# Kernel optimization log

Hardware: AMD Instinct MI355X
Metric: run time of the kernel (lower is better)

## Reference

```python
import jax, jax.numpy as jnp
import numpy as np
from jax import lax

B, D, H, W = 4, 64, 64, 64
CH = 150


def setup_inputs() -> dict:
    key = jax.random.key(0)
    k1, k2, k3, k4 = jax.random.split(key, 4)
    image = jax.random.uniform(k1, (B, 2, D, H, W), dtype=jnp.float32)
    # PyTorch-like init scales
    h_w = jax.random.normal(k2, (CH, 1, 3, 3, 3), dtype=jnp.float32) * (1.0 / np.sqrt(27.0))
    h_b = jax.random.normal(k3, (CH,), dtype=jnp.float32) * 0.05
    p_w = jax.random.normal(k4, (1, CH, 1, 1, 1), dtype=jnp.float32) * (1.0 / np.sqrt(CH))
    return {"image": image, "h_w": h_w, "h_b": h_b, "p_w": p_w, "k": 30}


def _max_pool3(v):
    # 3x3x3 max pool, stride 1, padding 1 (torch pads with -inf for max pool)
    return lax.reduce_window(
        v, -jnp.inf, lax.max,
        window_dimensions=(1, 1, 3, 3, 3),
        window_strides=(1, 1, 1, 1, 1),
        padding=[(0, 0), (0, 0), (1, 1), (1, 1), (1, 1)])


def reference(image, h_w, h_b, p_w, k):
    x = image[:, 0:1]            # [B,1,D,H,W] occupancy
    r = image[:, 1:2]            # [B,1,D,H,W] reward
    h = lax.conv_general_dilated(
        x, h_w, window_strides=(1, 1, 1), padding="SAME",
        dimension_numbers=("NCDHW", "OIDHW", "NCDHW"))
    h = jax.nn.relu(h + h_b[None, :, None, None, None])  # [B,150,D,H,W]
    # 1x1x1 conv == channel contraction
    p = jax.nn.sigmoid(jnp.einsum("bcdhw,c->bdhw", h, p_w[0, :, 0, 0, 0])[:, None])
    v = r
    for _ in range(k):
        v = jnp.maximum(v, r + p * (_max_pool3(v) - r))
    return v
```

## Files before the change

kernel.cpp:

```cpp
#include <hip/hip_runtime.h>
#include <math.h>

#define NEG_INF (-__builtin_inff())

typedef __attribute__((ext_vector_type(8))) short short8;
typedef __attribute__((ext_vector_type(4))) float f32x4;

__device__ __forceinline__ unsigned f2bf(float f) {
    union { float f; unsigned u; } v; v.f = f;
    return (v.u + 0x7fffu + ((v.u >> 16) & 1u)) >> 16;
}

__device__ __forceinline__ float dpp_shr1(float x) {
    return __int_as_float(__builtin_amdgcn_update_dpp(
        0, __float_as_int(x), 0x111, 0xF, 0xF, true));
}
__device__ __forceinline__ float dpp_shl1(float x) {
    return __int_as_float(__builtin_amdgcn_update_dpp(
        0, __float_as_int(x), 0x101, 0xF, 0xF, true));
}

__global__ __launch_bounds__(256) void pad_kernel(
    const float* __restrict__ img, unsigned short* __restrict__ pad)
{
    int i = blockIdx.x * 256 + threadIdx.x;
    if (i >= 66 * 66 * 66) return;
    int b = blockIdx.y;
    int z = i / 4356;
    int rem = i - z * 4356;
    int y = rem / 66;
    int x = rem - y * 66;
    float v = 0.f;
    if (z >= 1 && z <= 64 && y >= 1 && y <= 64 && x >= 1 && x <= 64)
        v = img[((size_t)b << 19) + ((z - 1) << 12) + ((y - 1) << 6) + (x - 1)];
    pad[(size_t)b * 287496 + i] = (unsigned short)f2bf(v);
}

__global__ __launch_bounds__(256, 2) void gate_mfma(
    const unsigned short* __restrict__ pad,
    const float* __restrict__ hw, const float* __restrict__ hb,
    const float* __restrict__ pw, float* __restrict__ p)
{
    const int lane = threadIdx.x & 63;
    const int col  = lane & 15;
    const int q    = lane >> 4;
    const int W    = blockIdx.x * 4 + (threadIdx.x >> 6);

    int4  bfrag[10];
    float pwv[10];
    #pragma unroll
    for (int t = 0; t < 10; ++t) {
        int c = 16 * t + col;
        bool cv = c < 150;
        unsigned hv[8];
        #pragma unroll
        for (int j = 0; j < 8; ++j) {
            int k = 8 * q + j;
            float wv = 0.f;
            if (cv) {
                if (k < 27) wv = hw[c * 27 + k];
                else if (k == 27) wv = hb[c];
            }
            hv[j] = f2bf(wv);
        }
        bfrag[t] = make_int4(hv[0] | (hv[1] << 16), hv[2] | (hv[3] << 16),
                             hv[4] | (hv[5] << 16), hv[6] | (hv[7] << 16));
        pwv[t] = cv ? pw[c] : 0.f;
    }

    int offL[8]; unsigned cstA[8]; bool ldA[8];
    #pragma unroll
    for (int j = 0; j < 8; ++j) {
        int k = 8 * q + j;
        int dz = (k * 57) >> 9;
        int rem = k - 9 * dz;
        int dy = (rem * 171) >> 9;
        int dx = rem - 3 * dy;
        ldA[j]  = (k < 27);
        offL[j] = (k < 27) ? (dz * 4356 + dy * 66 + dx) : 0;
        cstA[j] = (k == 27) ? 0x3F80u : 0u;
    }

    for (int i = 0; i < 16; ++i) {
        int g   = W * 16 + i;
        int x0  = (g & 3) << 4;
        int row = g >> 2;
        int y = row & 63, zz = (row >> 6) & 63, b = row >> 12;
        int abase = b * 287496 + zz * 4356 + y * 66 + x0 + col;

        unsigned av[8];
        #pragma unroll
        for (int j = 0; j < 8; ++j) {
            unsigned v = pad[abase + offL[j]];
            av[j] = ldA[j] ? v : cstA[j];
        }
        union { int4 i4; short8 s8; } af, bfu;
        af.i4 = make_int4(av[0] | (av[1] << 16), av[2] | (av[3] << 16),
                          av[4] | (av[5] << 16), av[6] | (av[7] << 16));

        const f32x4 zero = {0.f, 0.f, 0.f, 0.f};
        f32x4 rr[10];
        #pragma unroll
        for (int t = 0; t < 10; ++t) {
            bfu.i4 = bfrag[t];
            rr[t] = __builtin_amdgcn_mfma_f32_16x16x32_bf16(af.s8, bfu.s8, zero, 0, 0, 0);
        }
        float ax = 0.f, ay = 0.f, az = 0.f, aw = 0.f;
        #pragma unroll
        for (int t = 0; t < 10; ++t) {
            ax = fmaf(pwv[t], fmaxf(rr[t].x, 0.f), ax);
            ay = fmaf(pwv[t], fmaxf(rr[t].y, 0.f), ay);
            az = fmaf(pwv[t], fmaxf(rr[t].z, 0.f), az);
            aw = fmaf(pwv[t], fmaxf(rr[t].w, 0.f), aw);
        }
        #pragma unroll
        for (int m = 1; m < 16; m <<= 1) {
            ax += __shfl_xor(ax, m);
            ay += __shfl_xor(ay, m);
            az += __shfl_xor(az, m);
            aw += __shfl_xor(aw, m);
        }
        if (col == 0) {
            float4 o;
            o.x = 1.f / (1.f + __expf(-ax));
            o.y = 1.f / (1.f + __expf(-ay));
            o.z = 1.f / (1.f + __expf(-az));
            o.w = 1.f / (1.f + __expf(-aw));
            *(float4*)(p + (b << 18) + (zz << 12) + (y << 6) + x0 + 4 * q) = o;
        }
    }
}

#define ZC 12
#define YC 16
#define PL 1024
#define ZMID 6

template<int T>
__global__ __launch_bounds__(512, 4) void prop_kernel(
    const float* __restrict__ vin, int sstride,
    const float* __restrict__ rimg,
    const float* __restrict__ pbuf,
    float* __restrict__ vout)
{
    __shared__ float S[ZC * PL];
    int blk = blockIdx.x;
    int b  = blk >> 7;
    int tz = ((blk >> 3) & 15) << 2;
    int ty = (blk & 7) << 3;

    const float* vb = vin  + (size_t)b * sstride;
    const float* rb = rimg + ((size_t)b << 19);
    const float* pb = pbuf + ((size_t)b << 18);
    float*       ob = vout + ((size_t)b << 18);

    int tid  = threadIdx.x;
    int x4   = tid & 15, x0 = x4 << 2;
    int yy   = (tid >> 4) & 15;
    int h    = tid >> 8;
    int lane = tid & 63;
    (void)lane;

    int gy = ty + yy - 4;
    bool vy = (unsigned)gy < 64u;

    {
        const float* src = vb + gy * 64 + x0;
        #pragma unroll
        for (int zi = 0; zi < 6; ++zi) {
            int z  = 6 * h + zi;
            int gz = tz + z - 4;
            float4 v = make_float4(NEG_INF, NEG_INF, NEG_INF, NEG_INF);
            if (vy && ((unsigned)gz < 64u)) v = *(const float4*)(src + (gz << 12));
            *(float4*)(S + z * PL + yy * 64 + x0) = v;
        }
    }
    __syncthreads();

    int lbase = yy * 64 + x0;
    int goff  = gy * 64 + x0;

    #define ROWY(zz_, Q, C) {                                                  \
        const float* pz = S + (zz_) * PL + lbase;                              \
        float4 r0 = *(const float4*)(pz - 64);                                 \
        float4 r1 = *(const float4*)(pz);                                      \
        float4 r2 = *(const float4*)(pz + 64);                                 \
        float4 cm;                                                             \
        cm.x = fmaxf(fmaxf(r0.x, r1.x), r2.x);                                 \
        cm.y = fmaxf(fmaxf(r0.y, r1.y), r2.y);                                 \
        cm.z = fmaxf(fmaxf(r0.z, r1.z), r2.z);                                 \
        cm.w = fmaxf(fmaxf(r0.w, r1.w), r2.w);                                 \
        float lm = dpp_shr1(cm.w);                        \
        float rm = dpp_shl1(cm.x);                        \
        if (x4 == 0)  lm = NEG_INF;                                            \
        if (x4 == 15) rm = NEG_INF;                                            \
        Q.x = fmaxf(lm, fmaxf(cm.x, cm.y));                                    \
        Q.y = fmaxf(cm.x, fmaxf(cm.y, cm.z));                                  \
        Q.z = fmaxf(cm.y, fmaxf(cm.z, cm.w));                                  \
        Q.w = fmaxf(fmaxf(cm.z, cm.w), rm);                                    \
        C = r1;                                                                \
    }

    #pragma unroll
    for (int it = 0; it < T; ++it) {
        const int lo   = 5 - T + it;
        const int span = ZMID - lo;
        bool act = (yy >= lo) && (yy < YC - lo);
        int zlo = h ? ZMID : lo;
        float4 vn[5];
        if (act) {
            float4 q0, q1, q2, c1, c2, cd;
            ROWY(zlo - 1, q0, cd);
            ROWY(zlo,     q1, c1);
            #pragma unroll
            for (int zi = 0; zi < span; ++zi) {
                int z = zlo + zi;
                ROWY(z + 1, q2, c2);
                int gz = tz + z - 4;
                float4 r;
                if (vy && ((unsigned)gz < 64u)) {
                    int off = (gz << 12) + goff;
                    float4 pv = *(const float4*)(pb + off);
                    float4 rv = *(const float4*)(rb + off);
                    float4 m3;
                    m3.x = fmaxf(fmaxf(q0.x, q1.x), q2.x);
                    m3.y = fmaxf(fmaxf(q0.y, q1.y), q2.y);
                    m3.z = fmaxf(fmaxf(q0.z, q1.z), q2.z);
                    m3.w = fmaxf(fmaxf(q0.w, q1.w), q2.w);
                    r.x = fmaxf(c1.x, fmaf(pv.x, m3.x - rv.x, rv.x));
                    r.y = fmaxf(c1.y, fmaf(pv.y, m3.y - rv.y, rv.y));
                    r.z = fmaxf(c1.z, fmaf(pv.z, m3.z - rv.z, rv.z));
                    r.w = fmaxf(c1.w, fmaf(pv.w, m3.w - rv.w, rv.w));
                    if (it == T - 1) *(float4*)(ob + off) = r;
                } else {
                    r = c1;
                }
                vn[zi] = r;
                q0 = q1; q1 = q2; c1 = c2;
            }
        }
        __syncthreads();
        if (act) {
            #pragma unroll
            for (int zi = 0; zi < span; ++zi)
                *(float4*)(S + (zlo + zi) * PL + lbase) = vn[zi];
        }
        __syncthreads();
    }
    #undef ROWY
}

extern "C" void kernel_launch(void* const* d_in, const int* in_sizes, int n_in,
                              void* d_out, int out_size, void* d_ws, size_t ws_size,
                              hipStream_t stream) {
    const float* img = (const float*)d_in[0];
    const float* hw  = (const float*)d_in[1];
    const float* hb  = (const float*)d_in[2];
    const float* pw  = (const float*)d_in[3];

    float* out = (float*)d_out;
    float* p   = (float*)d_ws;
    float* vA  = (float*)((char*)d_ws + (4u << 20));
    unsigned short* pad = (unsigned short*)((char*)d_ws + (4u << 20));

    pad_kernel<<<dim3(1124, 4), 256, 0, stream>>>(img, pad);
    gate_mfma<<<1024, 256, 0, stream>>>(pad, hw, hb, pw, p);

    const float* r0 = img + (1 << 18);

    prop_kernel<4><<<512, 512, 0, stream>>>(r0,  1 << 19, r0, p, vA);
    prop_kernel<4><<<512, 512, 0, stream>>>(vA,  1 << 18, r0, p, out);
    prop_kernel<4><<<512, 512, 0, stream>>>(out, 1 << 18, r0, p, vA);
    prop_kernel<4><<<512, 512, 0, stream>>>(vA,  1 << 18, r0, p, out);
    prop_kernel<4><<<512, 512, 0, stream>>>(out, 1 << 18, r0, p, vA);
    prop_kernel<4><<<512, 512, 0, stream>>>(vA,  1 << 18, r0, p, out);
    prop_kernel<4><<<512, 512, 0, stream>>>(out, 1 << 18, r0, p, vA);
    prop_kernel<2><<<512, 512, 0, stream>>>(vA,  1 << 18, r0, p, out);
}
```

Before: 204.8 us.

## Spread gate kernel over more blocks, share weight prep via LDS, use DPP reductions

The gate MFMA kernel now assigns one output row per wave (four 16-wide tiles) and launches four times as many blocks with a higher occupancy hint. The bf16 weight fragments are built once per block, split across the waves, and exchanged through shared memory instead of every wave building all ten. The 16-lane reduction of the channel sum switches from shfl_xor to a DPP shift-right chain, and the result is written by lane 15. This aims to cut per-wave setup cost and shuffle latency and to raise parallelism, at the price of an extra barrier and LDS traffic per block.

```diff
diff --git a/kernel.cpp b/kernel.cpp
--- a/kernel.cpp
+++ b/kernel.cpp
@@ -14,6 +14,18 @@
 __device__ __forceinline__ float dpp_shr1(float x) {
     return __int_as_float(__builtin_amdgcn_update_dpp(
         0, __float_as_int(x), 0x111, 0xF, 0xF, true));
+}
+__device__ __forceinline__ float dpp_shr2(float x) {
+    return __int_as_float(__builtin_amdgcn_update_dpp(
+        0, __float_as_int(x), 0x112, 0xF, 0xF, true));
+}
+__device__ __forceinline__ float dpp_shr4(float x) {
+    return __int_as_float(__builtin_amdgcn_update_dpp(
+        0, __float_as_int(x), 0x114, 0xF, 0xF, true));
+}
+__device__ __forceinline__ float dpp_shr8(float x) {
+    return __int_as_float(__builtin_amdgcn_update_dpp(
+        0, __float_as_int(x), 0x118, 0xF, 0xF, true));
 }
 __device__ __forceinline__ float dpp_shl1(float x) {
     return __int_as_float(__builtin_amdgcn_update_dpp(
@@ -36,20 +48,20 @@
     pad[(size_t)b * 287496 + i] = (unsigned short)f2bf(v);
 }
 
-__global__ __launch_bounds__(256, 2) void gate_mfma(
+__global__ __launch_bounds__(256, 4) void gate_mfma(
     const unsigned short* __restrict__ pad,
     const float* __restrict__ hw, const float* __restrict__ hb,
     const float* __restrict__ pw, float* __restrict__ p)
 {
+    __shared__ int4 Bsh[10 * 64];
+
     const int lane = threadIdx.x & 63;
     const int col  = lane & 15;
     const int q    = lane >> 4;
-    const int W    = blockIdx.x * 4 + (threadIdx.x >> 6);
-
-    int4  bfrag[10];
-    float pwv[10];
-    #pragma unroll
-    for (int t = 0; t < 10; ++t) {
+    const int wid  = threadIdx.x >> 6;
+    const int W    = blockIdx.x * 4 + wid;
+
+    for (int t = wid; t < 10; t += 4) {
         int c = 16 * t + col;
         bool cv = c < 150;
         unsigned hv[8];
@@ -63,10 +75,20 @@
             }
             hv[j] = f2bf(wv);
         }
-        bfrag[t] = make_int4(hv[0] | (hv[1] << 16), hv[2] | (hv[3] << 16),
-                             hv[4] | (hv[5] << 16), hv[6] | (hv[7] << 16));
-        pwv[t] = cv ? pw[c] : 0.f;
-    }
+        Bsh[t * 64 + lane] = make_int4(hv[0] | (hv[1] << 16), hv[2] | (hv[3] << 16),
+                                       hv[4] | (hv[5] << 16), hv[6] | (hv[7] << 16));
+    }
+    float pwv[10];
+    #pragma unroll
+    for (int t = 0; t < 10; ++t) {
+        int c = 16 * t + col;
+        pwv[t] = (c < 150) ? pw[c] : 0.f;
+    }
+    __syncthreads();
+
+    int4 bfrag[10];
+    #pragma unroll
+    for (int t = 0; t < 10; ++t) bfrag[t] = Bsh[t * 64 + lane];
 
     int offL[8]; unsigned cstA[8]; bool ldA[8];
     #pragma unroll
@@ -81,12 +103,13 @@
         cstA[j] = (k == 27) ? 0x3F80u : 0u;
     }
 
-    for (int i = 0; i < 16; ++i) {
-        int g   = W * 16 + i;
-        int x0  = (g & 3) << 4;
-        int row = g >> 2;
-        int y = row & 63, zz = (row >> 6) & 63, b = row >> 12;
-        int abase = b * 287496 + zz * 4356 + y * 66 + x0 + col;
+    int y = W & 63, zz = (W >> 6) & 63, b = W >> 12;
+    int rbase = b * 287496 + zz * 4356 + y * 66 + col;
+
+    #pragma unroll 2
+    for (int i = 0; i < 4; ++i) {
+        int x0    = i << 4;
+        int abase = rbase + x0;
 
         unsigned av[8];
         #pragma unroll
@@ -113,14 +136,11 @@
             az = fmaf(pwv[t], fmaxf(rr[t].z, 0.f), az);
             aw = fmaf(pwv[t], fmaxf(rr[t].w, 0.f), aw);
         }
-        #pragma unroll
-        for (int m = 1; m < 16; m <<= 1) {
-            ax += __shfl_xor(ax, m);
-            ay += __shfl_xor(ay, m);
-            az += __shfl_xor(az, m);
-            aw += __shfl_xor(aw, m);
-        }
-        if (col == 0) {
+        ax += dpp_shr1(ax); ax += dpp_shr2(ax); ax += dpp_shr4(ax); ax += dpp_shr8(ax);
+        ay += dpp_shr1(ay); ay += dpp_shr2(ay); ay += dpp_shr4(ay); ay += dpp_shr8(ay);
+        az += dpp_shr1(az); az += dpp_shr2(az); az += dpp_shr4(az); az += dpp_shr8(az);
+        aw += dpp_shr1(aw); aw += dpp_shr2(aw); aw += dpp_shr4(aw); aw += dpp_shr8(aw);
+        if (col == 15) {
             float4 o;
             o.x = 1.f / (1.f + __expf(-ax));
             o.y = 1.f / (1.f + __expf(-ay));
@@ -264,7 +284,7 @@
     unsigned short* pad = (unsigned short*)((char*)d_ws + (4u << 20));
 
     pad_kernel<<<dim3(1124, 4), 256, 0, stream>>>(img, pad);
-    gate_mfma<<<1024, 256, 0, stream>>>(pad, hw, hb, pw, p);
+    gate_mfma<<<4096, 256, 0, stream>>>(pad, hw, hb, pw, p);
 
     const float* r0 = img + (1 << 18);
 
```

After: 203.9 us. About the same (-0.4%).
